# Kernel optimization log

Measured on AMD Instinct MI355X. Metric: run time of the kernel, lower is better.

Reference implementation:

```python
import jax, jax.numpy as jnp
import numpy as np

N = 40000       # nodes
E = 400000      # directed edges (before self-loops)
F_IN = 50       # PPI num_features
HID = 64        # per-head hidden
H = 4           # heads
NCLS = 121      # PPI num_classes
NEG_SLOPE = 0.2


def gat_layer(x, src, dst, W, a_src, a_dst, W_res, b, concat):
    """PyG GATConv: per-edge attention, segment softmax over dst, scatter-add."""
    n = x.shape[0]
    h, c = a_src.shape
    feat = (x @ W).reshape(n, h, c)                       # [N,H,C]
    al_s = (feat * a_src[None]).sum(-1)                   # [N,H]
    al_d = (feat * a_dst[None]).sum(-1)                   # [N,H]
    e = jax.nn.leaky_relu(al_s[src] + al_d[dst], NEG_SLOPE)  # [E,H]
    m = jax.ops.segment_max(e, dst, num_segments=n)       # stable softmax max
    e = jnp.exp(e - m[dst])
    denom = jax.ops.segment_sum(e, dst, num_segments=n)
    w = e / (denom[dst] + 1e-16)                          # [E,H] attention
    msg = feat[src] * w[:, :, None]                       # [E,H,C]
    out = jax.ops.segment_sum(msg, dst, num_segments=n)   # [N,H,C]
    out = out.reshape(n, h * c) if concat else out.mean(axis=1)
    return out + x @ W_res + b                            # residual proj + bias


def setup_inputs() -> dict:
    key = jax.random.key(0)
    ks = jax.random.split(key, 18)
    g = lambda k, shape: jax.random.normal(k, shape, dtype=jnp.float32) * 0.1
    return {
        "x": jax.random.normal(ks[0], (N, F_IN), dtype=jnp.float32),
        "edge_index": jax.random.randint(ks[1], (2, E), 0, N, dtype=jnp.int32),
        "W1": g(ks[2], (F_IN, H * HID)), "a1s": g(ks[3], (H, HID)), "a1d": g(ks[4], (H, HID)),
        "Wr1": g(ks[5], (F_IN, H * HID)), "b1": jnp.zeros((H * HID,), jnp.float32),
        "W2": g(ks[6], (H * HID, H * HID)), "a2s": g(ks[7], (H, HID)), "a2d": g(ks[8], (H, HID)),
        "Wr2": g(ks[9], (H * HID, H * HID)), "b2": jnp.zeros((H * HID,), jnp.float32),
        "W3": g(ks[10], (H * HID, H * NCLS)), "a3s": g(ks[11], (H, NCLS)), "a3d": g(ks[12], (H, NCLS)),
        "Wr3": g(ks[13], (H * HID, NCLS)), "b3": jnp.zeros((NCLS,), jnp.float32),
    }


def reference(x, edge_index, W1, a1s, a1d, Wr1, b1, W2, a2s, a2d, Wr2, b2,
              W3, a3s, a3d, Wr3, b3):
    loop = jnp.arange(N, dtype=edge_index.dtype)          # add_self_loops=True
    src = jnp.concatenate([edge_index[0], loop])
    dst = jnp.concatenate([edge_index[1], loop])
    h = jax.nn.relu(gat_layer(x, src, dst, W1, a1s, a1d, Wr1, b1, True))
    h = jax.nn.relu(gat_layer(h, src, dst, W2, a2s, a2d, Wr2, b2, True))
    return gat_layer(h, src, dst, W3, a3s, a3d, Wr3, b3, False)
```

## Files before the change

### kernel.cpp

```cpp
#include <hip/hip_runtime.h>
#include <hip/hip_bf16.h>


#define NNODES 40000
#define MPAD   40064
#define NEDGES 400000
#define FIN    50
#define NHEAD  4
#define SCANB  157
#define N4     160000

typedef __attribute__((ext_vector_type(8))) short short8;
typedef __attribute__((ext_vector_type(4))) float float4v;
typedef __attribute__((ext_vector_type(2))) float float2v;
typedef __attribute__((ext_vector_type(4))) unsigned short ushort4v;
typedef __attribute__((ext_vector_type(8))) unsigned short ushort8v;
typedef __attribute__((ext_vector_type(4))) unsigned int uint4v;

__device__ inline unsigned short f2bf(float f) {
    union { float f; unsigned u; } v; v.f = f;
    unsigned r = v.u + 0x7fff + ((v.u >> 16) & 1);
    return (unsigned short)(r >> 16);
}
__device__ inline float bf2f(unsigned short u) {
    union { unsigned u; float f; } v; v.u = ((unsigned)u) << 16; return v.f;
}
__device__ inline float lrelu(float x) { return x >= 0.f ? x : 0.2f * x; }

typedef __attribute__((address_space(3))) unsigned int lds_u32;
typedef __attribute__((address_space(1))) const unsigned int glb_u32;
__device__ __forceinline__ void gl2lds16(const short* g, short* l) {
    __builtin_amdgcn_global_load_lds((glb_u32*)g, (lds_u32*)l, 16, 0, 0);
}

__global__ void hist_kernel(const int* __restrict__ dst, int* __restrict__ counts, int E) {
    int i = blockIdx.x * blockDim.x + threadIdx.x;
    if (i < E) atomicAdd(&counts[dst[i]], 1);
}

__global__ __launch_bounds__(256) void scan_local(const int* __restrict__ counts,
                                                  int* __restrict__ offsets,
                                                  int* __restrict__ partials) {
    __shared__ int sh[256];
    int b = blockIdx.x, t = threadIdx.x, i = b * 256 + t;
    int v = (i < NNODES) ? counts[i] : 0;
    sh[t] = v;
    __syncthreads();
    #pragma unroll
    for (int off = 1; off < 256; off <<= 1) {
        int u = (t >= off) ? sh[t - off] : 0;
        __syncthreads();
        sh[t] += u;
        __syncthreads();
    }
    if (i < NNODES) offsets[i] = sh[t] - v;
    if (t == 255) partials[b] = sh[255];
}

__global__ __launch_bounds__(256) void scan_partials(int* __restrict__ partials,
                                                     int* __restrict__ pexcl) {
    __shared__ int sh[256];
    int t = threadIdx.x;
    int v = (t < SCANB) ? partials[t] : 0;
    sh[t] = v;
    __syncthreads();
    #pragma unroll
    for (int off = 1; off < 256; off <<= 1) {
        int u = (t >= off) ? sh[t - off] : 0;
        __syncthreads();
        sh[t] += u;
        __syncthreads();
    }
    pexcl[t] = sh[t] - v;
}

__global__ __launch_bounds__(256) void scan_carry(int* __restrict__ offsets,
                                                  const int* __restrict__ pexcl) {
    int b = blockIdx.x, i = b * 256 + threadIdx.x;
    if (i < NNODES) offsets[i] += pexcl[b];
}

__global__ void scatter_kernel(const int* __restrict__ src, const int* __restrict__ dst,
                               int* __restrict__ offsets,
                               int* __restrict__ csr_src, int* __restrict__ csr_dst, int E) {
    int i = blockIdx.x * blockDim.x + threadIdx.x;
    if (i < E) {
        int d = dst[i];
        int pos = atomicAdd(&offsets[d], 1);
        csr_src[pos] = src[i];
        csr_dst[pos] = d;
    }
}

__global__ void edge_p(const float* __restrict__ al4,
                       const int* __restrict__ csr_src, const int* __restrict__ csr_dst,
                       float* __restrict__ p4, int E) {
    int j = blockIdx.x * blockDim.x + threadIdx.x;
    if (j >= E) return;
    int s = csr_src[j], d = csr_dst[j];
    float4v a0 = *(const float4v*)&al4[s * 4];
    float4v a1 = *(const float4v*)&al4[2 * N4 + s * 4];
    float4v b0 = *(const float4v*)&al4[N4 + d * 4];
    float4v b1 = *(const float4v*)&al4[3 * N4 + d * 4];
    float4v p;
    p.x = __expf(lrelu(a0.x + a1.x + b0.x + b1.x));
    p.y = __expf(lrelu(a0.y + a1.y + b0.y + b1.y));
    p.z = __expf(lrelu(a0.z + a1.z + b0.z + b1.z));
    p.w = __expf(lrelu(a0.w + a1.w + b0.w + b1.w));
    *(float4v*)&p4[(size_t)j * 4] = p;
}

__global__ void convert_x(const float* __restrict__ x, short* __restrict__ xb) {
    int i = blockIdx.x * blockDim.x + threadIdx.x;
    if (i >= MPAD * 64) return;
    int r = i >> 6, k = i & 63;
    float v = (r < NNODES && k < FIN) ? x[r * FIN + k] : 0.f;
    xb[i] = f2bf(v);
}

__global__ void convert_pack1(const float* __restrict__ W1, const float* __restrict__ Wr1,
                              const float* __restrict__ W2, const float* __restrict__ Wr2,
                              short* __restrict__ wc1, short* __restrict__ wc2) {
    int i = blockIdx.x * blockDim.x + threadIdx.x;
    if (i < 32768) {
        const float* W = (i < 16384) ? W1 : Wr1;
        int j = i & 16383;
        int n = j >> 6, k = j & 63;
        wc1[i] = f2bf((k < FIN) ? W[k * 256 + n] : 0.f);
    } else if (i < 163840) {
        int j = (i - 32768) & 65535;
        const float* W = (i < 98304) ? W2 : Wr2;
        int n = j >> 8, k = j & 255;
        wc2[(i - 32768)] = f2bf(W[k * 256 + n]);
    }
}

__global__ void convert_pack2(const float* __restrict__ W3, const float* __restrict__ Wr3,
                              const float* __restrict__ a3s, const float* __restrict__ a3d,
                              short* __restrict__ wc3,
                              float* __restrict__ a3sp, float* __restrict__ a3dp) {
    int i = blockIdx.x * blockDim.x + threadIdx.x;
    if (i < 131072) {
        int j = i >> 8, k = i & 255;
        int h = j >> 7, c = j & 127;
        wc3[i] = f2bf((c < 121) ? W3[k * 484 + h * 121 + c] : 0.f);
    } else if (i < 163840) {
        int j = i - 131072;
        int n = j >> 8, k = j & 255;
        wc3[131072 + j] = f2bf((n < 121) ? Wr3[k * 121 + n] : 0.f);
    } else if (i < 164864) {
        int j = i - 163840;
        int which = j >> 9; int jj = j & 511;
        int h = jj >> 7, c = jj & 127;
        float v = (c < 121) ? (which ? a3d[h * 121 + c] : a3s[h * 121 + c]) : 0.f;
        (which ? a3dp : a3sp)[jj] = v;
    }
}

__global__ void convert_f8(const unsigned short* __restrict__ Fb, unsigned int* __restrict__ F8) {
    int i = blockIdx.x * blockDim.x + threadIdx.x;
    if (i >= NNODES * 128) return;
    ushort4v f = *(const ushort4v*)&Fb[(size_t)i * 4];
    int v = 0;
    v = __builtin_amdgcn_cvt_pk_fp8_f32(bf2f(f.x), bf2f(f.y), v, false);
    v = __builtin_amdgcn_cvt_pk_fp8_f32(bf2f(f.z), bf2f(f.w), v, true);
    F8[i] = (unsigned int)v;
}

template<int MODE>
__global__ __launch_bounds__(256) void mfma_gemm_fused(const short* __restrict__ A,
                                                       const short* __restrict__ Bt,
                                                       const float* __restrict__ bias,
                                                       const float* __restrict__ asv,
                                                       const float* __restrict__ adv,
                                                       unsigned short* __restrict__ Fb,
                                                       unsigned short* __restrict__ Rb,
                                                       float* __restrict__ out,
                                                       float* __restrict__ al4,
                                                       int Kp) {
    const int NW  = MODE ? 512 : 256;
    const int NCB = MODE ? 5 : 4;
    __shared__ __align__(16) short AsBs[16384];
    __shared__ __align__(16) unsigned short Cs[2][32][132];
    short* As = AsBs;
    short* Bs = AsBs + 8192;

    const int tid = threadIdx.x;
    const int l   = tid & 63;
    const int w   = tid >> 6;
    const int wm  = w >> 1, wn = w & 1;
    const int lrow = l & 15;
    const int lq   = l >> 4;

    const int T = NCB * 313;
    const int flat = blockIdx.y * NCB + blockIdx.x;
    const int q8 = T >> 3, r8 = T & 7;
    const int xcd = flat & 7, sidx = flat >> 3;
    const int wg = (xcd < r8 ? xcd * (q8 + 1) : r8 * (q8 + 1) + (xcd - r8) * q8) + sidx;
    const int row0 = (wg / NCB) * 128;
    const int col0 = (wg % NCB) * 128;

    float4v acc[4][4] = {};

    const int lr_ld = tid >> 3;
    const int lk_ld = (tid & 7) * 8;
    const int nk = Kp >> 6;
    for (int t = 0; t < nk; ++t) {
        const int k0 = t << 6;
        if (t) __syncthreads();
        const size_t abase = (size_t)(row0 + lr_ld) * Kp + k0 + lk_ld;
        const size_t bbase = (size_t)(col0 + lr_ld) * Kp + k0 + lk_ld;
        #pragma unroll
        for (int j = 0; j < 4; ++j) {
            gl2lds16(&A[abase + (size_t)j * 32 * Kp],  &As[j * 2048 + tid * 8]);
            gl2lds16(&Bt[bbase + (size_t)j * 32 * Kp], &Bs[j * 2048 + tid * 8]);
        }
        __syncthreads();
        #pragma unroll
        for (int ks = 0; ks < 2; ++ks) {
            short8 aF[4], bF[4];
            #pragma unroll
            for (int rt = 0; rt < 4; ++rt)
                aF[rt] = *(const short8*)&As[(wm * 64 + rt * 16 + lrow) * 64 + ks * 32 + lq * 8];
            #pragma unroll
            for (int ct = 0; ct < 4; ++ct)
                bF[ct] = *(const short8*)&Bs[(wn * 64 + ct * 16 + lrow) * 64 + ks * 32 + lq * 8];
            #pragma unroll
            for (int rt = 0; rt < 4; ++rt)
                #pragma unroll
                for (int ct = 0; ct < 4; ++ct)
                    acc[rt][ct] = __builtin_amdgcn_mfma_f32_16x16x32_bf16(aF[rt], bF[ct],
                                                                          acc[rt][ct], 0, 0, 0);
        }
    }

    const int colbase = col0 + wn * 64;
    const bool isW = colbase < NW;

    if (isW) {
        const int head = (colbase * NHEAD) / NW;
        const int half = MODE ? ((colbase >> 6) & 1) : 0;
        float* als_o = al4 + (half ? 2 * N4 : 0);
        float* ald_o = als_o + N4;
        float as_c[4], ad_c[4];
        #pragma unroll
        for (int ct = 0; ct < 4; ++ct) {
            int col = colbase + ct * 16 + lrow;
            as_c[ct] = asv[col];
            ad_c[ct] = adv[col];
        }
        #pragma unroll
        for (int rt = 0; rt < 4; ++rt) {
            #pragma unroll
            for (int i = 0; i < 4; ++i) {
                int r = row0 + wm * 64 + rt * 16 + lq * 4 + i;
                float fs = 0.f, fd = 0.f;
                #pragma unroll
                for (int ct = 0; ct < 4; ++ct) {
                    float v = acc[rt][ct][i];
                    fs += v * as_c[ct];
                    fd += v * ad_c[ct];
                }
                #pragma unroll
                for (int o2 = 8; o2; o2 >>= 1) {
                    fs += __shfl_xor(fs, o2, 16);
                    fd += __shfl_xor(fd, o2, 16);
                }
                if (lrow == 0 && r < NNODES) {
                    als_o[r * 4 + head] = fs;
                    ald_o[r * 4 + head] = fd;
                }
            }
        }
    }

    if (MODE == 1 && col0 >= 512) {
        float* Ls = (float*)AsBs;
        #pragma unroll
        for (int p = 0; p < 4; ++p) {
            __syncthreads();
            if (wm == (p >> 1)) {
                const int rt0 = (p & 1) * 2;
                #pragma unroll
                for (int rt2 = 0; rt2 < 2; ++rt2) {
                    int rt = rt0 + rt2;
                    #pragma unroll
                    for (int ct = 0; ct < 4; ++ct) {
                        int cl = wn * 64 + ct * 16 + lrow;
                        #pragma unroll
                        for (int i = 0; i < 4; ++i) {
                            int lr = rt2 * 16 + lq * 4 + i;
                            Ls[lr * 132 + cl] = acc[rt][ct][i];
                        }
                    }
                }
            }
            __syncthreads();
            #pragma unroll
            for (int it = 0; it < 16; ++it) {
                int idx = it * 256 + tid;
                int r = idx >> 7, c = idx & 127;
                int grow = row0 + p * 32 + r;
                if (c < 121 && grow < NNODES)
                    out[(size_t)grow * 121 + c] = Ls[r * 132 + c] + bias[c];
            }
        }
        return;
    }

    const bool isRb = (MODE == 0) && (col0 >= 256);
    unsigned short* dest = isRb ? Rb : Fb;
    const int ldd = MODE ? 512 : 256;
    const int cold = isRb ? col0 - 256 : col0;
    float badd[4] = {0.f, 0.f, 0.f, 0.f};
    if (isRb) {
        #pragma unroll
        for (int ct = 0; ct < 4; ++ct)
            badd[ct] = bias[col0 - 256 + wn * 64 + ct * 16 + lrow];
    }

    const int rp = tid >> 2, g = rp >> 5, rr = rp & 31, qq = tid & 3;
    #pragma unroll
    for (int p = 0; p < 2; ++p) {
        if (p) __syncthreads();
        #pragma unroll
        for (int rt2 = 0; rt2 < 2; ++rt2) {
            int rt = p * 2 + rt2;
            #pragma unroll
            for (int ct = 0; ct < 4; ++ct) {
                int cl = wn * 64 + ct * 16 + lrow;
                #pragma unroll
                for (int i = 0; i < 4; ++i) {
                    int lr = rt2 * 16 + lq * 4 + i;
                    Cs[wm][lr][cl] = f2bf(acc[rt][ct][i] + badd[ct]);
                }
            }
        }
        __syncthreads();
        int grow = row0 + g * 64 + p * 32 + rr;
        if (grow < NNODES) {
            #pragma unroll
            for (int k = 0; k < 4; ++k) {
                ushort8v v = *(const ushort8v*)&Cs[g][rr][qq * 32 + 8 * k];
                *(ushort8v*)&dest[(size_t)grow * ldd + cold + qq * 32 + 8 * k] = v;
            }
        }
    }
}

__global__ __launch_bounds__(256) void attn64_kernel(const unsigned short* __restrict__ featb,
                                                     const float* __restrict__ al4,
                                                     const int* __restrict__ offs,
                                                     const int* __restrict__ csr,
                                                     const float* __restrict__ p4,
                                                     const unsigned short* __restrict__ Rb,
                                                     unsigned short* __restrict__ outb) {
    int n = blockIdx.x * 4 + (threadIdx.x >> 6);
    int l = threadIdx.x & 63;
    int half = l >> 5, li = l & 31;
    int h = li >> 3;
    int beg = n ? offs[n - 1] : 0;
    int end = offs[n];

    float a[8] = {};
    float s = 0.f;
    #pragma unroll 4
    for (int j = beg + half; j < end; j += 2) {
        int sn = csr[j];
        float p = p4[(size_t)j * 4 + h];
        s += p;
        ushort8v f = *(const ushort8v*)&featb[(size_t)sn * 256 + 8 * li];
        #pragma unroll
        for (int i = 0; i < 8; ++i) a[i] += p * bf2f(f[i]);
    }
    s += __shfl_xor(s, 32, 64);
    #pragma unroll
    for (int i = 0; i < 8; ++i) a[i] += __shfl_xor(a[i], 32, 64);

    float lg = al4[n * 4 + h] + al4[2 * N4 + n * 4 + h]
             + al4[N4 + n * 4 + h] + al4[3 * N4 + n * 4 + h];
    float p0 = __expf(lrelu(lg));
    s += p0;
    {
        ushort8v f = *(const ushort8v*)&featb[(size_t)n * 256 + 8 * li];
        #pragma unroll
        for (int i = 0; i < 8; ++i) a[i] += p0 * bf2f(f[i]);
    }
    if (half == 0) {
        float inv = 1.f / s;
        ushort8v r = *(const ushort8v*)&Rb[(size_t)n * 256 + 8 * li];
        ushort8v o;
        #pragma unroll
        for (int i = 0; i < 8; ++i) o[i] = f2bf(fmaxf(bf2f(r[i]) + a[i] * inv, 0.f));
        *(ushort8v*)&outb[(size_t)n * 256 + 8 * li] = o;
    }
}

__global__ __launch_bounds__(256) void attn121_kernel(const unsigned int* __restrict__ F8,
                                                      const float* __restrict__ al4,
                                                      const int* __restrict__ offs,
                                                      const int* __restrict__ csr,
                                                      const float* __restrict__ p4,
                                                      float* __restrict__ out) {
    int n = blockIdx.x * 4 + (threadIdx.x >> 6);
    int l = threadIdx.x & 63;
    int half = l >> 5, li = l & 31;
    int h = li >> 3;
    int beg = n ? offs[n - 1] : 0;
    int end = offs[n];

    float a[16] = {};
    float s = 0.f;
    #pragma unroll 2
    for (int j = beg + half; j < end; j += 2) {
        int sn = csr[j];
        float p = p4[(size_t)j * 4 + h];
        s += p;
        uint4v u = *(const uint4v*)&F8[(size_t)sn * 128 + 4 * li];
        #pragma unroll
        for (int k = 0; k < 4; ++k) {
            float2v lo = __builtin_amdgcn_cvt_pk_f32_fp8(u[k], false);
            float2v hi = __builtin_amdgcn_cvt_pk_f32_fp8(u[k], true);
            a[4 * k + 0] += p * lo.x; a[4 * k + 1] += p * lo.y;
            a[4 * k + 2] += p * hi.x; a[4 * k + 3] += p * hi.y;
        }
    }
    s += __shfl_xor(s, 32, 64);
    #pragma unroll
    for (int i = 0; i < 16; ++i) a[i] += __shfl_xor(a[i], 32, 64);

    float lg = al4[n * 4 + h] + al4[2 * N4 + n * 4 + h]
             + al4[N4 + n * 4 + h] + al4[3 * N4 + n * 4 + h];
    float p0 = __expf(lrelu(lg));
    s += p0;
    {
        uint4v u = *(const uint4v*)&F8[(size_t)n * 128 + 4 * li];
        #pragma unroll
        for (int k = 0; k < 4; ++k) {
            float2v lo = __builtin_amdgcn_cvt_pk_f32_fp8(u[k], false);
            float2v hi = __builtin_amdgcn_cvt_pk_f32_fp8(u[k], true);
            a[4 * k + 0] += p0 * lo.x; a[4 * k + 1] += p0 * lo.y;
            a[4 * k + 2] += p0 * hi.x; a[4 * k + 3] += p0 * hi.y;
        }
    }
    float inv = 0.25f / s;
    #pragma unroll
    for (int i = 0; i < 16; ++i) {
        a[i] *= inv;
        a[i] += __shfl_xor(a[i], 8, 64);
        a[i] += __shfl_xor(a[i], 16, 64);
    }
    if (l < 8) {
        #pragma unroll
        for (int i = 0; i < 16; ++i) {
            int c = 16 * l + i;
            if (c < 121) out[(size_t)n * 121 + c] += a[i];
        }
    }
}

extern "C" void kernel_launch(void* const* d_in, const int* in_sizes, int n_in,
                              void* d_out, int out_size, void* d_ws, size_t ws_size,
                              hipStream_t stream) {
    const float* x   = (const float*)d_in[0];
    const int* ei    = (const int*)d_in[1];
    const float* W1  = (const float*)d_in[2];
    const float* a1s = (const float*)d_in[3];
    const float* a1d = (const float*)d_in[4];
    const float* Wr1 = (const float*)d_in[5];
    const float* b1  = (const float*)d_in[6];
    const float* W2  = (const float*)d_in[7];
    const float* a2s = (const float*)d_in[8];
    const float* a2d = (const float*)d_in[9];
    const float* Wr2 = (const float*)d_in[10];
    const float* b2  = (const float*)d_in[11];
    const float* W3  = (const float*)d_in[12];
    const float* a3s = (const float*)d_in[13];
    const float* a3d = (const float*)d_in[14];
    const float* Wr3 = (const float*)d_in[15];
    const float* b3  = (const float*)d_in[16];
    float* out = (float*)d_out;

    const int* e_src = ei;
    const int* e_dst = ei + NEDGES;

    char* ws = (char*)d_ws;
    size_t off = 0;
    auto carve = [&](size_t bytes) { void* p = ws + off; off += (bytes + 255) & ~255ull; return p; };
    unsigned short* Fb = (unsigned short*)carve((size_t)MPAD * 512 * 2);
    unsigned short* Rb = (unsigned short*)carve((size_t)MPAD * 256 * 2);
    unsigned short* Hb = (unsigned short*)carve((size_t)MPAD * 256 * 2);
    unsigned int* F8 = (unsigned int*)carve((size_t)NNODES * 128 * 4);
    short* xb   = (short*)carve((size_t)MPAD * 64 * 2);
    short* wc1  = (short*)carve((size_t)512 * 64 * 2);
    short* wc2  = (short*)carve((size_t)512 * 256 * 2);
    short* wc3  = (short*)carve((size_t)640 * 256 * 2);
    float* a3sp = (float*)carve(512 * 4);
    float* a3dp = (float*)carve(512 * 4);
    float* al4  = (float*)carve((size_t)4 * N4 * 4);
    float* p4   = (float*)carve((size_t)NEDGES * 4 * 4);
    int* csr_src = (int*)carve((size_t)NEDGES * 4);
    int* csr_dst = (int*)carve((size_t)NEDGES * 4);
    int* offsets = (int*)carve(((size_t)NNODES + 4) * 4);
    int* counts  = (int*)carve((size_t)NNODES * 4);
    int* partials = (int*)carve(256 * 4);
    int* pexcl    = (int*)carve(256 * 4);

    const int EB = (NEDGES + 255) / 256;
    dim3 blk(256);

    convert_x<<<(MPAD * 64 + 255) / 256, blk, 0, stream>>>(x, xb);
    convert_pack1<<<(163840 + 255) / 256, blk, 0, stream>>>(W1, Wr1, W2, Wr2, wc1, wc2);
    convert_pack2<<<(164864 + 255) / 256, blk, 0, stream>>>(W3, Wr3, a3s, a3d, wc3, a3sp, a3dp);

    hipMemsetAsync(al4 + 2 * N4, 0, (size_t)2 * N4 * 4, stream);

    hipMemsetAsync(counts, 0, NNODES * 4, stream);
    hist_kernel<<<EB, blk, 0, stream>>>(e_dst, counts, NEDGES);
    scan_local<<<SCANB, blk, 0, stream>>>(counts, offsets, partials);
    scan_partials<<<1, blk, 0, stream>>>(partials, pexcl);
    scan_carry<<<SCANB, blk, 0, stream>>>(offsets, pexcl);
    scatter_kernel<<<EB, blk, 0, stream>>>(e_src, e_dst, offsets, csr_src, csr_dst, NEDGES);

    mfma_gemm_fused<0><<<dim3(4, 313), blk, 0, stream>>>(xb, wc1, b1, a1s, a1d,
                                                         Fb, Rb, nullptr, al4, 64);
    edge_p<<<EB, blk, 0, stream>>>(al4, csr_src, csr_dst, p4, NEDGES);
    attn64_kernel<<<NNODES / 4, blk, 0, stream>>>(Fb, al4, offsets, csr_src, p4, Rb, Hb);

    mfma_gemm_fused<0><<<dim3(4, 313), blk, 0, stream>>>((short*)Hb, wc2, b2, a2s, a2d,
                                                         Fb, Rb, nullptr, al4, 256);
    edge_p<<<EB, blk, 0, stream>>>(al4, csr_src, csr_dst, p4, NEDGES);
    attn64_kernel<<<NNODES / 4, blk, 0, stream>>>(Fb, al4, offsets, csr_src, p4, Rb, Hb);

    mfma_gemm_fused<1><<<dim3(5, 313), blk, 0, stream>>>((short*)Hb, wc3, b3, a3sp, a3dp,
                                                         Fb, nullptr, out, al4, 256);
    convert_f8<<<(NNODES * 128 + 255) / 256, blk, 0, stream>>>(Fb, F8);
    edge_p<<<EB, blk, 0, stream>>>(al4, csr_src, csr_dst, p4, NEDGES);
    attn121_kernel<<<NNODES / 4, blk, 0, stream>>>(F8, al4, offsets, csr_src, p4, out);
}
```

Measured before the change: 427.1 us.

## Double-buffer A tiles in LDS, load B directly to registers, swizzle LDS

Reworks the GEMM main loop so the A tile is double-buffered in shared memory and the next tile is prefetched while MFMAs run on the current one. The B operand is read straight from global memory into registers, one tile ahead, instead of being staged through LDS. An XOR swizzle on the LDS column index is meant to avoid bank conflicts, and launch bounds request 3 blocks per CU. The cost is more registers for the B prefetch and uncoalesced per-lane global reads of B. The GEMM is only part of the total time, which also covers the edge softmax and scatter kernels.

```diff
diff --git a/kernel.cpp b/kernel.cpp
--- a/kernel.cpp
+++ b/kernel.cpp
@@ -168,22 +168,20 @@
 }
 
 template<int MODE>
-__global__ __launch_bounds__(256) void mfma_gemm_fused(const short* __restrict__ A,
-                                                       const short* __restrict__ Bt,
-                                                       const float* __restrict__ bias,
-                                                       const float* __restrict__ asv,
-                                                       const float* __restrict__ adv,
-                                                       unsigned short* __restrict__ Fb,
-                                                       unsigned short* __restrict__ Rb,
-                                                       float* __restrict__ out,
-                                                       float* __restrict__ al4,
-                                                       int Kp) {
+__global__ __launch_bounds__(256, 3) void mfma_gemm_fused(const short* __restrict__ A,
+                                                          const short* __restrict__ Bt,
+                                                          const float* __restrict__ bias,
+                                                          const float* __restrict__ asv,
+                                                          const float* __restrict__ adv,
+                                                          unsigned short* __restrict__ Fb,
+                                                          unsigned short* __restrict__ Rb,
+                                                          float* __restrict__ out,
+                                                          float* __restrict__ al4,
+                                                          int Kp) {
     const int NW  = MODE ? 512 : 256;
     const int NCB = MODE ? 5 : 4;
-    __shared__ __align__(16) short AsBs[16384];
+    __shared__ __align__(16) short As[2][8192];
     __shared__ __align__(16) unsigned short Cs[2][32][132];
-    short* As = AsBs;
-    short* Bs = AsBs + 8192;
 
     const int tid = threadIdx.x;
     const int l   = tid & 63;
@@ -203,35 +201,53 @@
     float4v acc[4][4] = {};
 
     const int lr_ld = tid >> 3;
-    const int lk_ld = (tid & 7) * 8;
+    const int lk_ld = ((tid & 7) ^ (lr_ld & 7)) * 8;
     const int nk = Kp >> 6;
+
+    const int bcol = col0 + wn * 64 + lrow;
+
+    short8 bc[8], bn[8];
+
+    #pragma unroll
+    for (int j = 0; j < 4; ++j)
+        gl2lds16(&A[(size_t)(row0 + j * 32 + lr_ld) * Kp + lk_ld],
+                 &As[0][j * 2048 + tid * 8]);
+    #pragma unroll
+    for (int ks = 0; ks < 2; ++ks)
+        #pragma unroll
+        for (int ct = 0; ct < 4; ++ct)
+            bc[ks * 4 + ct] = *(const short8*)&Bt[(size_t)(bcol + ct * 16) * Kp + ks * 32 + lq * 8];
+    __syncthreads();
+
     for (int t = 0; t < nk; ++t) {
-        const int k0 = t << 6;
-        if (t) __syncthreads();
-        const size_t abase = (size_t)(row0 + lr_ld) * Kp + k0 + lk_ld;
-        const size_t bbase = (size_t)(col0 + lr_ld) * Kp + k0 + lk_ld;
-        #pragma unroll
-        for (int j = 0; j < 4; ++j) {
-            gl2lds16(&A[abase + (size_t)j * 32 * Kp],  &As[j * 2048 + tid * 8]);
-            gl2lds16(&Bt[bbase + (size_t)j * 32 * Kp], &Bs[j * 2048 + tid * 8]);
-        }
-        __syncthreads();
-        #pragma unroll
-        for (int ks = 0; ks < 2; ++ks) {
-            short8 aF[4], bF[4];
-            #pragma unroll
-            for (int rt = 0; rt < 4; ++rt)
-                aF[rt] = *(const short8*)&As[(wm * 64 + rt * 16 + lrow) * 64 + ks * 32 + lq * 8];
-            #pragma unroll
-            for (int ct = 0; ct < 4; ++ct)
-                bF[ct] = *(const short8*)&Bs[(wn * 64 + ct * 16 + lrow) * 64 + ks * 32 + lq * 8];
-            #pragma unroll
-            for (int rt = 0; rt < 4; ++rt)
+        if (t + 1 < nk) {
+            const int k1 = (t + 1) << 6;
+            #pragma unroll
+            for (int j = 0; j < 4; ++j)
+                gl2lds16(&A[(size_t)(row0 + j * 32 + lr_ld) * Kp + k1 + lk_ld],
+                         &As[(t + 1) & 1][j * 2048 + tid * 8]);
+            #pragma unroll
+            for (int ks = 0; ks < 2; ++ks)
                 #pragma unroll
                 for (int ct = 0; ct < 4; ++ct)
-                    acc[rt][ct] = __builtin_amdgcn_mfma_f32_16x16x32_bf16(aF[rt], bF[ct],
+                    bn[ks * 4 + ct] = *(const short8*)&Bt[(size_t)(bcol + ct * 16) * Kp + k1 + ks * 32 + lq * 8];
+        }
+        const short* Ab = As[t & 1];
+        #pragma unroll
+        for (int ks = 0; ks < 2; ++ks) {
+            #pragma unroll
+            for (int rt = 0; rt < 4; ++rt) {
+                short8 aF = *(const short8*)&Ab[(wm * 64 + rt * 16 + lrow) * 64
+                                                + ((((ks << 2) | lq)) ^ (lrow & 7)) * 8];
+                #pragma unroll
+                for (int ct = 0; ct < 4; ++ct)
+                    acc[rt][ct] = __builtin_amdgcn_mfma_f32_16x16x32_bf16(aF, bc[ks * 4 + ct],
                                                                           acc[rt][ct], 0, 0, 0);
-        }
+            }
+        }
+        __syncthreads();
+        #pragma unroll
+        for (int i = 0; i < 8; ++i) bc[i] = bn[i];
     }
 
     const int colbase = col0 + wn * 64;
@@ -275,7 +291,7 @@
     }
 
     if (MODE == 1 && col0 >= 512) {
-        float* Ls = (float*)AsBs;
+        float* Ls = (float*)As;
         #pragma unroll
         for (int p = 0; p < 4; ++p) {
             __syncthreads();
```

New measurement: 439.3 us. 1.03x slower.

## Stage full-K A tile in swizzled LDS and stream B from registers in GEMM

Applied to the files above, without the earlier changes.

The GEMM now loads the whole 128xK A tile into LDS once, with an XOR swizzle against bank conflicts, instead of looping over K in 64-wide chunks with a sync per chunk. B fragments are read straight from global memory into registers and double-buffered across K chunks. K becomes a template parameter and launch bounds ask for 2 blocks per CU. The K-loop barriers go away, but LDS per block grows to 64KB for K=256, which may cap occupancy, and B is no longer shared between waves through LDS, so global and L2 traffic for B rises.

```diff
diff --git a/kernel.cpp b/kernel.cpp
--- a/kernel.cpp
+++ b/kernel.cpp
@@ -167,23 +167,30 @@
     F8[i] = (unsigned int)v;
 }
 
-template<int MODE>
-__global__ __launch_bounds__(256) void mfma_gemm_fused(const short* __restrict__ A,
-                                                       const short* __restrict__ Bt,
-                                                       const float* __restrict__ bias,
-                                                       const float* __restrict__ asv,
-                                                       const float* __restrict__ adv,
-                                                       unsigned short* __restrict__ Fb,
-                                                       unsigned short* __restrict__ Rb,
-                                                       float* __restrict__ out,
-                                                       float* __restrict__ al4,
-                                                       int Kp) {
+template<int MODE, int KP>
+__global__ __launch_bounds__(256, 2) void mfma_gemm_fused(const short* __restrict__ A,
+                                                          const short* __restrict__ Bt,
+                                                          const float* __restrict__ bias,
+                                                          const float* __restrict__ asv,
+                                                          const float* __restrict__ adv,
+                                                          unsigned short* __restrict__ Fb,
+                                                          unsigned short* __restrict__ Rb,
+                                                          float* __restrict__ out,
+                                                          float* __restrict__ al4) {
     const int NW  = MODE ? 512 : 256;
     const int NCB = MODE ? 5 : 4;
-    __shared__ __align__(16) short AsBs[16384];
-    __shared__ __align__(16) unsigned short Cs[2][32][132];
-    short* As = AsBs;
-    short* Bs = AsBs + 8192;
+    constexpr int GPR  = KP / 8;
+    constexpr int LG2  = (KP == 256) ? 5 : 3;
+    constexpr int NLD  = (128 * GPR) / 256;
+    constexpr int NKS  = KP / 32;
+    constexpr int CH   = (NKS >= 4) ? 2 : 1;
+    constexpr int NCH  = NKS / CH;
+    constexpr unsigned ABYTES = 128u * KP * 2u;
+    constexpr unsigned SBYTES = (ABYTES > 16896u) ? ABYTES : 16896u;
+    __shared__ __align__(16) char smem[SBYTES];
+    short* As = (short*)smem;
+    auto Cs = (unsigned short (*)[32][132])smem;
+    float* Ls = (float*)smem;
 
     const int tid = threadIdx.x;
     const int l   = tid & 63;
@@ -202,36 +209,51 @@
 
     float4v acc[4][4] = {};
 
-    const int lr_ld = tid >> 3;
-    const int lk_ld = (tid & 7) * 8;
-    const int nk = Kp >> 6;
-    for (int t = 0; t < nk; ++t) {
-        const int k0 = t << 6;
-        if (t) __syncthreads();
-        const size_t abase = (size_t)(row0 + lr_ld) * Kp + k0 + lk_ld;
-        const size_t bbase = (size_t)(col0 + lr_ld) * Kp + k0 + lk_ld;
-        #pragma unroll
-        for (int j = 0; j < 4; ++j) {
-            gl2lds16(&A[abase + (size_t)j * 32 * Kp],  &As[j * 2048 + tid * 8]);
-            gl2lds16(&Bt[bbase + (size_t)j * 32 * Kp], &Bs[j * 2048 + tid * 8]);
-        }
-        __syncthreads();
-        #pragma unroll
-        for (int ks = 0; ks < 2; ++ks) {
-            short8 aF[4], bF[4];
-            #pragma unroll
-            for (int rt = 0; rt < 4; ++rt)
-                aF[rt] = *(const short8*)&As[(wm * 64 + rt * 16 + lrow) * 64 + ks * 32 + lq * 8];
+    #pragma unroll
+    for (int j = 0; j < NLD; ++j) {
+        int G   = j * 256 + tid;
+        int row = G >> LG2;
+        int pg  = G & (GPR - 1);
+        int lg  = pg ^ (row & 7);
+        gl2lds16(&A[(size_t)(row0 + row) * KP + lg * 8], &As[(size_t)G * 8]);
+    }
+
+    const int bcol = col0 + wn * 64 + lrow;
+    short8 bA[CH * 4], bB[CH * 4];
+
+    auto loadB = [&](int c, short8* buf) {
+        #pragma unroll
+        for (int ks2 = 0; ks2 < CH; ++ks2)
             #pragma unroll
             for (int ct = 0; ct < 4; ++ct)
-                bF[ct] = *(const short8*)&Bs[(wn * 64 + ct * 16 + lrow) * 64 + ks * 32 + lq * 8];
+                buf[ks2 * 4 + ct] = *(const short8*)
+                    &Bt[(size_t)(bcol + ct * 16) * KP + (c * CH + ks2) * 32 + lq * 8];
+    };
+    auto computeC = [&](int c, short8* buf) {
+        #pragma unroll
+        for (int ks2 = 0; ks2 < CH; ++ks2) {
+            const int g = (c * CH + ks2) * 4 + lq;
             #pragma unroll
-            for (int rt = 0; rt < 4; ++rt)
+            for (int rt = 0; rt < 4; ++rt) {
+                short8 aF = *(const short8*)
+                    &As[(wm * 64 + rt * 16 + lrow) * KP + (g ^ (lrow & 7)) * 8];
                 #pragma unroll
                 for (int ct = 0; ct < 4; ++ct)
-                    acc[rt][ct] = __builtin_amdgcn_mfma_f32_16x16x32_bf16(aF[rt], bF[ct],
+                    acc[rt][ct] = __builtin_amdgcn_mfma_f32_16x16x32_bf16(aF, buf[ks2 * 4 + ct],
                                                                           acc[rt][ct], 0, 0, 0);
-        }
+            }
+        }
+    };
+
+    loadB(0, bA);
+    __syncthreads();
+
+    #pragma unroll
+    for (int c = 0; c < NCH; ++c) {
+        short8* cur = (c & 1) ? bB : bA;
+        short8* nxt = (c & 1) ? bA : bB;
+        if (c + 1 < NCH) loadB(c + 1, nxt);
+        computeC(c, cur);
     }
 
     const int colbase = col0 + wn * 64;
@@ -275,7 +297,6 @@
     }
 
     if (MODE == 1 && col0 >= 512) {
-        float* Ls = (float*)AsBs;
         #pragma unroll
         for (int p = 0; p < 4; ++p) {
             __syncthreads();
@@ -319,10 +340,10 @@
             badd[ct] = bias[col0 - 256 + wn * 64 + ct * 16 + lrow];
     }
 
-    const int rp = tid >> 2, g = rp >> 5, rr = rp & 31, qq = tid & 3;
+    const int rp = tid >> 2, g2 = rp >> 5, rr = rp & 31, qq = tid & 3;
     #pragma unroll
     for (int p = 0; p < 2; ++p) {
-        if (p) __syncthreads();
+        __syncthreads();
         #pragma unroll
         for (int rt2 = 0; rt2 < 2; ++rt2) {
             int rt = p * 2 + rt2;
@@ -337,11 +358,11 @@
             }
         }
         __syncthreads();
-        int grow = row0 + g * 64 + p * 32 + rr;
+        int grow = row0 + g2 * 64 + p * 32 + rr;
         if (grow < NNODES) {
             #pragma unroll
             for (int k = 0; k < 4; ++k) {
-                ushort8v v = *(const ushort8v*)&Cs[g][rr][qq * 32 + 8 * k];
+                ushort8v v = *(const ushort8v*)&Cs[g2][rr][qq * 32 + 8 * k];
                 *(ushort8v*)&dest[(size_t)grow * ldd + cold + qq * 32 + 8 * k] = v;
             }
         }
@@ -522,18 +543,18 @@
     scan_carry<<<SCANB, blk, 0, stream>>>(offsets, pexcl);
     scatter_kernel<<<EB, blk, 0, stream>>>(e_src, e_dst, offsets, csr_src, csr_dst, NEDGES);
 
-    mfma_gemm_fused<0><<<dim3(4, 313), blk, 0, stream>>>(xb, wc1, b1, a1s, a1d,
-                                                         Fb, Rb, nullptr, al4, 64);
+    mfma_gemm_fused<0, 64><<<dim3(4, 313), blk, 0, stream>>>(xb, wc1, b1, a1s, a1d,
+                                                             Fb, Rb, nullptr, al4);
     edge_p<<<EB, blk, 0, stream>>>(al4, csr_src, csr_dst, p4, NEDGES);
     attn64_kernel<<<NNODES / 4, blk, 0, stream>>>(Fb, al4, offsets, csr_src, p4, Rb, Hb);
 
-    mfma_gemm_fused<0><<<dim3(4, 313), blk, 0, stream>>>((short*)Hb, wc2, b2, a2s, a2d,
-                                                         Fb, Rb, nullptr, al4, 256);
+    mfma_gemm_fused<0, 256><<<dim3(4, 313), blk, 0, stream>>>((short*)Hb, wc2, b2, a2s, a2d,
+                                                              Fb, Rb, nullptr, al4);
     edge_p<<<EB, blk, 0, stream>>>(al4, csr_src, csr_dst, p4, NEDGES);
     attn64_kernel<<<NNODES / 4, blk, 0, stream>>>(Fb, al4, offsets, csr_src, p4, Rb, Hb);
 
-    mfma_gemm_fused<1><<<dim3(5, 313), blk, 0, stream>>>((short*)Hb, wc3, b3, a3sp, a3dp,
-                                                         Fb, nullptr, out, al4, 256);
+    mfma_gemm_fused<1, 256><<<dim3(5, 313), blk, 0, stream>>>((short*)Hb, wc3, b3, a3sp, a3dp,
+                                                              Fb, nullptr, out, al4);
     convert_f8<<<(NNODES * 128 + 255) / 256, blk, 0, stream>>>(Fb, F8);
     edge_p<<<EB, blk, 0, stream>>>(al4, csr_src, csr_dst, p4, NEDGES);
     attn121_kernel<<<NNODES / 4, blk, 0, stream>>>(F8, al4, offsets, csr_src, p4, out);
```

Result: slower. 447.1 us (+4.7%).

## Fuse edge score computation into attention kernels and FP8 packing into GEMM epilogue

Applied to the files above, without the earlier changes.

Drops the separate edge_p kernel and the p4 edge-weight buffer. Each attention kernel now computes exp(leaky_relu(src+dst logits)) inline from al4 per gathered edge, and csr_dst is no longer needed. The layer-3 GEMM epilogue writes FP8-packed features straight to F8, which removes the convert_f8 pass and the bf16 round trip through Fb. This saves several launches and large edge-sized memory passes, at the cost of an extra random gather and exp per edge in the attention loops. It also assumes layers 1 and 2 read only one al4 slot, so the removed memset must not matter.

```diff
diff --git a/kernel.cpp b/kernel.cpp
--- a/kernel.cpp
+++ b/kernel.cpp
@@ -15,6 +15,7 @@
 typedef __attribute__((ext_vector_type(2))) float float2v;
 typedef __attribute__((ext_vector_type(4))) unsigned short ushort4v;
 typedef __attribute__((ext_vector_type(8))) unsigned short ushort8v;
+typedef __attribute__((ext_vector_type(2))) unsigned int uint2v;
 typedef __attribute__((ext_vector_type(4))) unsigned int uint4v;
 
 __device__ inline unsigned short f2bf(float f) {
@@ -82,32 +83,13 @@
 
 __global__ void scatter_kernel(const int* __restrict__ src, const int* __restrict__ dst,
                                int* __restrict__ offsets,
-                               int* __restrict__ csr_src, int* __restrict__ csr_dst, int E) {
+                               int* __restrict__ csr_src, int E) {
     int i = blockIdx.x * blockDim.x + threadIdx.x;
     if (i < E) {
         int d = dst[i];
         int pos = atomicAdd(&offsets[d], 1);
         csr_src[pos] = src[i];
-        csr_dst[pos] = d;
-    }
-}
-
-__global__ void edge_p(const float* __restrict__ al4,
-                       const int* __restrict__ csr_src, const int* __restrict__ csr_dst,
-                       float* __restrict__ p4, int E) {
-    int j = blockIdx.x * blockDim.x + threadIdx.x;
-    if (j >= E) return;
-    int s = csr_src[j], d = csr_dst[j];
-    float4v a0 = *(const float4v*)&al4[s * 4];
-    float4v a1 = *(const float4v*)&al4[2 * N4 + s * 4];
-    float4v b0 = *(const float4v*)&al4[N4 + d * 4];
-    float4v b1 = *(const float4v*)&al4[3 * N4 + d * 4];
-    float4v p;
-    p.x = __expf(lrelu(a0.x + a1.x + b0.x + b1.x));
-    p.y = __expf(lrelu(a0.y + a1.y + b0.y + b1.y));
-    p.z = __expf(lrelu(a0.z + a1.z + b0.z + b1.z));
-    p.w = __expf(lrelu(a0.w + a1.w + b0.w + b1.w));
-    *(float4v*)&p4[(size_t)j * 4] = p;
+    }
 }
 
 __global__ void convert_x(const float* __restrict__ x, short* __restrict__ xb) {
@@ -157,16 +139,6 @@
     }
 }
 
-__global__ void convert_f8(const unsigned short* __restrict__ Fb, unsigned int* __restrict__ F8) {
-    int i = blockIdx.x * blockDim.x + threadIdx.x;
-    if (i >= NNODES * 128) return;
-    ushort4v f = *(const ushort4v*)&Fb[(size_t)i * 4];
-    int v = 0;
-    v = __builtin_amdgcn_cvt_pk_fp8_f32(bf2f(f.x), bf2f(f.y), v, false);
-    v = __builtin_amdgcn_cvt_pk_fp8_f32(bf2f(f.z), bf2f(f.w), v, true);
-    F8[i] = (unsigned int)v;
-}
-
 template<int MODE>
 __global__ __launch_bounds__(256) void mfma_gemm_fused(const short* __restrict__ A,
                                                        const short* __restrict__ Bt,
@@ -175,6 +147,7 @@
                                                        const float* __restrict__ adv,
                                                        unsigned short* __restrict__ Fb,
                                                        unsigned short* __restrict__ Rb,
+                                                       unsigned int* __restrict__ F8,
                                                        float* __restrict__ out,
                                                        float* __restrict__ al4,
                                                        int Kp) {
@@ -273,6 +246,8 @@
             }
         }
     }
+
+    const int rp = tid >> 2, g2 = rp >> 5, rr = rp & 31, qq = tid & 3;
 
     if (MODE == 1 && col0 >= 512) {
         float* Ls = (float*)AsBs;
@@ -308,9 +283,44 @@
         return;
     }
 
-    const bool isRb = (MODE == 0) && (col0 >= 256);
+    if (MODE == 1) {
+        #pragma unroll
+        for (int p = 0; p < 2; ++p) {
+            if (p) __syncthreads();
+            #pragma unroll
+            for (int rt2 = 0; rt2 < 2; ++rt2) {
+                int rt = p * 2 + rt2;
+                #pragma unroll
+                for (int ct = 0; ct < 4; ++ct) {
+                    int cl = wn * 64 + ct * 16 + lrow;
+                    #pragma unroll
+                    for (int i = 0; i < 4; ++i) {
+                        int lr = rt2 * 16 + lq * 4 + i;
+                        Cs[wm][lr][cl] = f2bf(acc[rt][ct][i]);
+                    }
+                }
+            }
+            __syncthreads();
+            int grow = row0 + g2 * 64 + p * 32 + rr;
+            if (grow < NNODES) {
+                #pragma unroll
+                for (int k = 0; k < 4; ++k) {
+                    ushort8v v = *(const ushort8v*)&Cs[g2][rr][qq * 32 + 8 * k];
+                    int u0 = 0, u1 = 0;
+                    u0 = __builtin_amdgcn_cvt_pk_fp8_f32(bf2f(v[0]), bf2f(v[1]), u0, false);
+                    u0 = __builtin_amdgcn_cvt_pk_fp8_f32(bf2f(v[2]), bf2f(v[3]), u0, true);
+                    u1 = __builtin_amdgcn_cvt_pk_fp8_f32(bf2f(v[4]), bf2f(v[5]), u1, false);
+                    u1 = __builtin_amdgcn_cvt_pk_fp8_f32(bf2f(v[6]), bf2f(v[7]), u1, true);
+                    uint2v wv; wv.x = (unsigned)u0; wv.y = (unsigned)u1;
+                    *(uint2v*)&F8[(size_t)grow * 128 + (col0 >> 2) + qq * 8 + 2 * k] = wv;
+                }
+            }
+        }
+        return;
+    }
+
+    const bool isRb = col0 >= 256;
     unsigned short* dest = isRb ? Rb : Fb;
-    const int ldd = MODE ? 512 : 256;
     const int cold = isRb ? col0 - 256 : col0;
     float badd[4] = {0.f, 0.f, 0.f, 0.f};
     if (isRb) {
@@ -319,7 +329,6 @@
             badd[ct] = bias[col0 - 256 + wn * 64 + ct * 16 + lrow];
     }
 
-    const int rp = tid >> 2, g = rp >> 5, rr = rp & 31, qq = tid & 3;
     #pragma unroll
     for (int p = 0; p < 2; ++p) {
         if (p) __syncthreads();
@@ -337,12 +346,12 @@
             }
         }
         __syncthreads();
-        int grow = row0 + g * 64 + p * 32 + rr;
+        int grow = row0 + g2 * 64 + p * 32 + rr;
         if (grow < NNODES) {
             #pragma unroll
             for (int k = 0; k < 4; ++k) {
-                ushort8v v = *(const ushort8v*)&Cs[g][rr][qq * 32 + 8 * k];
-                *(ushort8v*)&dest[(size_t)grow * ldd + cold + qq * 32 + 8 * k] = v;
+                ushort8v v = *(const ushort8v*)&Cs[g2][rr][qq * 32 + 8 * k];
+                *(ushort8v*)&dest[(size_t)grow * 256 + cold + qq * 32 + 8 * k] = v;
             }
         }
     }
@@ -352,7 +361,6 @@
                                                      const float* __restrict__ al4,
                                                      const int* __restrict__ offs,
                                                      const int* __restrict__ csr,
-                                                     const float* __restrict__ p4,
                                                      const unsigned short* __restrict__ Rb,
                                                      unsigned short* __restrict__ outb) {
     int n = blockIdx.x * 4 + (threadIdx.x >> 6);
@@ -361,13 +369,14 @@
     int h = li >> 3;
     int beg = n ? offs[n - 1] : 0;
     int end = offs[n];
+    float d0 = al4[N4 + n * 4 + h];
 
     float a[8] = {};
     float s = 0.f;
     #pragma unroll 4
     for (int j = beg + half; j < end; j += 2) {
         int sn = csr[j];
-        float p = p4[(size_t)j * 4 + h];
+        float p = __expf(lrelu(al4[sn * 4 + h] + d0));
         s += p;
         ushort8v f = *(const ushort8v*)&featb[(size_t)sn * 256 + 8 * li];
         #pragma unroll
@@ -377,9 +386,7 @@
     #pragma unroll
     for (int i = 0; i < 8; ++i) a[i] += __shfl_xor(a[i], 32, 64);
 
-    float lg = al4[n * 4 + h] + al4[2 * N4 + n * 4 + h]
-             + al4[N4 + n * 4 + h] + al4[3 * N4 + n * 4 + h];
-    float p0 = __expf(lrelu(lg));
+    float p0 = __expf(lrelu(al4[n * 4 + h] + d0));
     s += p0;
     {
         ushort8v f = *(const ushort8v*)&featb[(size_t)n * 256 + 8 * li];
@@ -400,7 +407,6 @@
                                                       const float* __restrict__ al4,
                                                       const int* __restrict__ offs,
                                                       const int* __restrict__ csr,
-                                                      const float* __restrict__ p4,
                                                       float* __restrict__ out) {
     int n = blockIdx.x * 4 + (threadIdx.x >> 6);
     int l = threadIdx.x & 63;
@@ -408,13 +414,14 @@
     int h = li >> 3;
     int beg = n ? offs[n - 1] : 0;
     int end = offs[n];
+    float dsum = al4[N4 + n * 4 + h] + al4[3 * N4 + n * 4 + h];
 
     float a[16] = {};
     float s = 0.f;
     #pragma unroll 2
     for (int j = beg + half; j < end; j += 2) {
         int sn = csr[j];
-        float p = p4[(size_t)j * 4 + h];
+        float p = __expf(lrelu(al4[sn * 4 + h] + al4[2 * N4 + sn * 4 + h] + dsum));
         s += p;
         uint4v u = *(const uint4v*)&F8[(size_t)sn * 128 + 4 * li];
         #pragma unroll
@@ -429,9 +436,7 @@
     #pragma unroll
     for (int i = 0; i < 16; ++i) a[i] += __shfl_xor(a[i], 32, 64);
 
-    float lg = al4[n * 4 + h] + al4[2 * N4 + n * 4 + h]
-             + al4[N4 + n * 4 + h] + al4[3 * N4 + n * 4 + h];
-    float p0 = __expf(lrelu(lg));
+    float p0 = __expf(lrelu(al4[n * 4 + h] + al4[2 * N4 + n * 4 + h] + dsum));
     s += p0;
     {
         uint4v u = *(const uint4v*)&F8[(size_t)n * 128 + 4 * li];
@@ -487,7 +492,7 @@
     char* ws = (char*)d_ws;
     size_t off = 0;
     auto carve = [&](size_t bytes) { void* p = ws + off; off += (bytes + 255) & ~255ull; return p; };
-    unsigned short* Fb = (unsigned short*)carve((size_t)MPAD * 512 * 2);
+    unsigned short* Fb = (unsigned short*)carve((size_t)MPAD * 256 * 2);
     unsigned short* Rb = (unsigned short*)carve((size_t)MPAD * 256 * 2);
     unsigned short* Hb = (unsigned short*)carve((size_t)MPAD * 256 * 2);
     unsigned int* F8 = (unsigned int*)carve((size_t)NNODES * 128 * 4);
@@ -498,9 +503,7 @@
     float* a3sp = (float*)carve(512 * 4);
     float* a3dp = (float*)carve(512 * 4);
     float* al4  = (float*)carve((size_t)4 * N4 * 4);
-    float* p4   = (float*)carve((size_t)NEDGES * 4 * 4);
     int* csr_src = (int*)carve((size_t)NEDGES * 4);
-    int* csr_dst = (int*)carve((size_t)NEDGES * 4);
     int* offsets = (int*)carve(((size_t)NNODES + 4) * 4);
     int* counts  = (int*)carve((size_t)NNODES * 4);
     int* partials = (int*)carve(256 * 4);
@@ -512,29 +515,23 @@
     convert_x<<<(MPAD * 64 + 255) / 256, blk, 0, stream>>>(x, xb);
     convert_pack1<<<(163840 + 255) / 256, blk, 0, stream>>>(W1, Wr1, W2, Wr2, wc1, wc2);
     convert_pack2<<<(164864 + 255) / 256, blk, 0, stream>>>(W3, Wr3, a3s, a3d, wc3, a3sp, a3dp);
-
-    hipMemsetAsync(al4 + 2 * N4, 0, (size_t)2 * N4 * 4, stream);
 
     hipMemsetAsync(counts, 0, NNODES * 4, stream);
     hist_kernel<<<EB, blk, 0, stream>>>(e_dst, counts, NEDGES);
     scan_local<<<SCANB, blk, 0, stream>>>(counts, offsets, partials);
     scan_partials<<<1, blk, 0, stream>>>(partials, pexcl);
     scan_carry<<<SCANB, blk, 0, stream>>>(offsets, pexcl);
-    scatter_kernel<<<EB, blk, 0, stream>>>(e_src, e_dst, offsets, csr_src, csr_dst, NEDGES);
+    scatter_kernel<<<EB, blk, 0, stream>>>(e_src, e_dst, offsets, csr_src, NEDGES);
 
     mfma_gemm_fused<0><<<dim3(4, 313), blk, 0, stream>>>(xb, wc1, b1, a1s, a1d,
-                                                         Fb, Rb, nullptr, al4, 64);
-    edge_p<<<EB, blk, 0, stream>>>(al4, csr_src, csr_dst, p4, NEDGES);
-    attn64_kernel<<<NNODES / 4, blk, 0, stream>>>(Fb, al4, offsets, csr_src, p4, Rb, Hb);
+                                                         Fb, Rb, nullptr, nullptr, al4, 64);
+    attn64_kernel<<<NNODES / 4, blk, 0, stream>>>(Fb, al4, offsets, csr_src, Rb, Hb);
 
     mfma_gemm_fused<0><<<dim3(4, 313), blk, 0, stream>>>((short*)Hb, wc2, b2, a2s, a2d,
-                                                         Fb, Rb, nullptr, al4, 256);
-    edge_p<<<EB, blk, 0, stream>>>(al4, csr_src, csr_dst, p4, NEDGES);
-    attn64_kernel<<<NNODES / 4, blk, 0, stream>>>(Fb, al4, offsets, csr_src, p4, Rb, Hb);
+                                                         Fb, Rb, nullptr, nullptr, al4, 256);
+    attn64_kernel<<<NNODES / 4, blk, 0, stream>>>(Fb, al4, offsets, csr_src, Rb, Hb);
 
     mfma_gemm_fused<1><<<dim3(5, 313), blk, 0, stream>>>((short*)Hb, wc3, b3, a3sp, a3dp,
-                                                         Fb, nullptr, out, al4, 256);
-    convert_f8<<<(NNODES * 128 + 255) / 256, blk, 0, stream>>>(Fb, F8);
-    edge_p<<<EB, blk, 0, stream>>>(al4, csr_src, csr_dst, p4, NEDGES);
-    attn121_kernel<<<NNODES / 4, blk, 0, stream>>>(F8, al4, offsets, csr_src, p4, out);
-}
+                                                         nullptr, nullptr, F8, out, al4, 256);
+    attn121_kernel<<<NNODES / 4, blk, 0, stream>>>(F8, al4, offsets, csr_src, out);
+}
```

Measured after the change: 384.4 us. 1.11x faster.
